# Optimization experiments

Measured on AMD Instinct MI355X. Metric: run time of the kernel, lower is better.

The kernel has to match this reference:

```python
import jax, jax.numpy as jnp
import numpy as np

N = 100000   # nodes
E = 1600000  # edges
IN = 41      # in_channels (21 atom + 20 residue)
ED = 8       # edge_dim
H = 64       # hidden_dim
L = 3        # num_layers
G = 256      # graphs in batch
ATOM = 21
EPS = 1e-5   # GraphNorm eps


def setup_inputs() -> dict:
    key = jax.random.key(0)
    ks = jax.random.split(key, 32)
    s = 0.1
    x = jax.random.normal(ks[0], (N, IN), jnp.float32)
    # make even-index nodes 'ligand' atoms (zero residue part) so both MLP branches fire
    lig = (jnp.arange(N) % 2) == 0
    x = x.at[:, ATOM:].set(jnp.where(lig[:, None], 0.0, x[:, ATOM:]))
    edge_index = jax.random.randint(ks[1], (2, E), 0, N)
    edge_attr = jax.random.normal(ks[2], (E, ED), jnp.float32)
    batch = jnp.sort(jax.random.randint(ks[3], (N,), 0, G))
    p = {
        "lig_W1": s * jax.random.normal(ks[4], (IN, H), jnp.float32),
        "lig_b1": jnp.zeros((H,), jnp.float32),
        "lig_W2": s * jax.random.normal(ks[5], (H, H), jnp.float32),
        "lig_b2": jnp.zeros((H,), jnp.float32),
        "prot_W1": s * jax.random.normal(ks[6], (IN, H), jnp.float32),
        "prot_b1": jnp.zeros((H,), jnp.float32),
        "prot_W2": s * jax.random.normal(ks[7], (H, H), jnp.float32),
        "prot_b2": jnp.zeros((H,), jnp.float32),
        # per-layer stacked params for the 3 GINEConv + GraphNorm blocks
        "conv_We": s * jax.random.normal(ks[8], (L, ED, H), jnp.float32),
        "conv_be": jnp.zeros((L, H), jnp.float32),
        "conv_W1": s * jax.random.normal(ks[9], (L, H, H), jnp.float32),
        "conv_b1": jnp.zeros((L, H), jnp.float32),
        "conv_W2": s * jax.random.normal(ks[10], (L, H, H), jnp.float32),
        "conv_b2": jnp.zeros((L, H), jnp.float32),
        "norm_w": jnp.ones((L, H), jnp.float32),
        "norm_b": jnp.zeros((L, H), jnp.float32),
        "norm_a": jnp.ones((L, H), jnp.float32),  # mean_scale alpha
        "out_W1": s * jax.random.normal(ks[11], (H, H), jnp.float32),
        "out_b1": jnp.zeros((H,), jnp.float32),
        "out_W2": s * jax.random.normal(ks[12], (H, 1), jnp.float32),
        "out_b2": jnp.zeros((1,), jnp.float32),
    }
    return dict(x=x, edge_index=edge_index, edge_attr=edge_attr, batch=batch, **p)


def reference(x, edge_index, edge_attr, batch,
              lig_W1, lig_b1, lig_W2, lig_b2,
              prot_W1, prot_b1, prot_W2, prot_b2,
              conv_We, conv_be, conv_W1, conv_b1, conv_W2, conv_b2,
              norm_w, norm_b, norm_a,
              out_W1, out_b1, out_W2, out_b2):
    # --- input encoder: ligand vs protein branch by residue-part mask ---
    res_mask = jnp.sum(jnp.abs(x[:, ATOM:]), axis=1) > 1e-6
    h_lig = jax.nn.relu(jax.nn.relu(x @ lig_W1 + lig_b1) @ lig_W2 + lig_b2)
    h_prot = jax.nn.relu(jax.nn.relu(x @ prot_W1 + prot_b1) @ prot_W2 + prot_b2)
    h = jnp.where(res_mask[:, None], h_prot, h_lig)  # [N, H]

    src, dst = edge_index[0], edge_index[1]
    counts = jnp.maximum(jax.ops.segment_sum(jnp.ones((N,), h.dtype), batch,
                                             num_segments=G), 1.0)[:, None]  # [G,1]

    for l in range(L):
        # GINEConv (eps=0): nn(h_i + sum_j relu(h_j + lin(e_ij)))
        e = edge_attr @ conv_We[l] + conv_be[l]           # [E, H]
        msg = jax.nn.relu(h[src] + e)                     # [E, H]
        aggr = jax.ops.segment_sum(msg, dst, num_segments=N)
        z = h + aggr
        h = jax.nn.relu(z @ conv_W1[l] + conv_b1[l]) @ conv_W2[l] + conv_b2[l]
        # GraphNorm: (h - alpha*mean_g) / sqrt(var_g + eps) * w + b
        mean = jax.ops.segment_sum(h, batch, num_segments=G) / counts  # [G, H]
        out = h - norm_a[l] * mean[batch]
        var = jax.ops.segment_sum(out * out, batch, num_segments=G) / counts
        h = norm_w[l] * (out / jnp.sqrt(var + EPS)[batch]) + norm_b[l]
        h = jax.nn.relu(h)

    # global_add_pool + readout (dropout = identity at eval)
    g = jax.ops.segment_sum(h, batch, num_segments=G)  # [G, H]
    out = jax.nn.relu(g @ out_W1 + out_b1) @ out_W2 + out_b2  # [G, 1]
    return out.reshape(-1)
```

## Files before the change

kernel.cpp:

```cpp
#include <hip/hip_runtime.h>

#define NN 100000
#define NE 1600000
#define IN_CH 41
#define EDIM 8
#define H 64
#define GNUM 256
#define ATOM 21
#define EPSV 1e-5f
#define EPW 16
#define NTILE (NN / 16)

#define BSH 7
#define BDST 128
#define NBK 782
#define GRP 16
#define BDST2 8
#define NAGG 12500
#define SCAP 3584

#define VPT_H 8
#define EPB_H (1024 * VPT_H)
#define NBLK_H ((NE + EPB_H - 1) / EPB_H)
#define VPT_P1 16
#define EPB_P1 (1024 * VPT_P1)
#define NBLK_P1 ((NE + EPB_P1 - 1) / EPB_P1)

typedef unsigned short u16;
typedef unsigned int u32;
typedef unsigned long long u64;
typedef __attribute__((ext_vector_type(8))) short short8;
typedef __attribute__((ext_vector_type(4))) float floatx4;

__device__ __forceinline__ u16 f2bf(float f) {
    u32 u = __float_as_uint(f);
    u32 r = (u + 0x7FFFu + ((u >> 16) & 1u)) >> 16;
    return (u16)r;
}
__device__ __forceinline__ float bf2f(u16 u) {
    return __uint_as_float(((u32)u) << 16);
}
__device__ __forceinline__ floatx4 mfma16(short8 a, short8 b, floatx4 c) {
    return __builtin_amdgcn_mfma_f32_16x16x32_bf16(a, b, c, 0, 0, 0);
}
__device__ __forceinline__ short8 pack_bf8(float4 a, float4 b) {
    short8 s;
    s[0] = (short)f2bf(a.x); s[1] = (short)f2bf(a.y);
    s[2] = (short)f2bf(a.z); s[3] = (short)f2bf(a.w);
    s[4] = (short)f2bf(b.x); s[5] = (short)f2bf(b.y);
    s[6] = (short)f2bf(b.z); s[7] = (short)f2bf(b.w);
    return s;
}

__global__ __launch_bounds__(256) void partition_kernel(
    const float* __restrict__ x, int* __restrict__ ctr,
    int* __restrict__ lig_list, int* __restrict__ prot_list)
{
    const int n = blockIdx.x * 256 + threadIdx.x;
    const int lane = threadIdx.x & 63;
    float m = 0.0f;
    if (n < NN) {
        const float* xr = x + (size_t)n * IN_CH + ATOM;
#pragma unroll
        for (int d = 0; d < IN_CH - ATOM; ++d) m += fabsf(xr[d]);
    }
    const bool valid = n < NN;
    const bool prot = valid && (m > 1e-6f);
    const bool lig = valid && !prot;

    const u64 bl = __ballot(lig);
    const u64 bp = __ballot(prot);
    const u64 below_m = (lane == 63) ? (~0ull >> 1) : ((1ull << lane) - 1ull);
    int base_l = 0, base_p = 0;
    if (lane == 0) {
        if (bl) base_l = atomicAdd(&ctr[0], (int)__popcll(bl));
        if (bp) base_p = atomicAdd(&ctr[1], (int)__popcll(bp));
    }
    base_l = __shfl(base_l, 0, 64);
    base_p = __shfl(base_p, 0, 64);
    if (lig)  lig_list [base_l + (int)__popcll(bl & below_m)] = n;
    if (prot) prot_list[base_p + (int)__popcll(bp & below_m)] = n;
}

__global__ __launch_bounds__(256) void xb_kernel(
    const float* __restrict__ x, u16* __restrict__ xb)
{
    const int id = blockIdx.x * 256 + threadIdx.x;
    if (id >= NN * H) return;
    const int n = id >> 6, d = id & 63;
    xb[id] = (d < IN_CH) ? f2bf(x[(size_t)n * IN_CH + d]) : (u16)0;
}

__global__ __launch_bounds__(256) void ea2b_kernel(
    const float* __restrict__ ea, uint4* __restrict__ eab16g)
{
    const int e = blockIdx.x * 256 + threadIdx.x;
    if (e >= NE) return;
    const float4* e4 = (const float4*)(ea + (size_t)e * EDIM);
    const float4 a = e4[0], b = e4[1];
    uint4 u;
    u.x = (u32)f2bf(a.x) | ((u32)f2bf(a.y) << 16);
    u.y = (u32)f2bf(a.z) | ((u32)f2bf(a.w) << 16);
    u.z = (u32)f2bf(b.x) | ((u32)f2bf(b.y) << 16);
    u.w = (u32)f2bf(b.z) | ((u32)f2bf(b.w) << 16);
    eab16g[e] = u;
}

__global__ __launch_bounds__(256) void prep_w_kernel(
    const float* __restrict__ ligW1, const float* __restrict__ ligW2,
    const float* __restrict__ protW1, const float* __restrict__ protW2,
    const float* __restrict__ convW1, const float* __restrict__ convW2,
    u16* __restrict__ wf)
{
    const int id = blockIdx.x * 256 + threadIdx.x;
    if (id >= 10 * 4096) return;
    const int j = id & 7, l = (id >> 3) & 63, t = (id >> 9) & 3;
    const int c = (id >> 11) & 1, mat = id >> 12;
    const int k = c * 32 + ((l >> 4) * 8) + j;
    const int n = t * 16 + (l & 15);
    const float* src; int K = 64;
    if (mat == 0)      { src = ligW1;  K = IN_CH; }
    else if (mat == 1) { src = ligW2; }
    else if (mat == 2) { src = protW1; K = IN_CH; }
    else if (mat == 3) { src = protW2; }
    else {
        const int layer = (mat - 4) >> 1;
        src = (((mat - 4) & 1) ? convW2 : convW1) + (size_t)layer * H * H;
    }
    wf[id] = (k < K) ? f2bf(src[(size_t)k * H + n]) : (u16)0;
}

__global__ __launch_bounds__(256) void enc_mfma_kernel(
    const int* __restrict__ list, const int* __restrict__ countPtr,
    const u16* __restrict__ xb,
    const u16* __restrict__ w1f, const u16* __restrict__ w2f,
    const float* __restrict__ bia1, const float* __restrict__ bia2,
    float* __restrict__ h, u16* __restrict__ h16)
{
    __shared__ __align__(16) u16 hid[4][16 * 72];
    const int wv = threadIdx.x >> 6;
    const int lane = threadIdx.x & 63;
    const int tile = blockIdx.x * 4 + wv;
    const int count = *countPtr;
    if (tile * 16 >= count) return;
    const int quad = lane >> 4;
    const int mi = lane & 15;
    int idx = tile * 16 + mi;
    if (idx >= count) idx = count - 1;
    const int nid = list[idx];

    const short8 a0 = *(const short8*)(xb + (size_t)nid * H + quad * 8);
    const short8 a1 = *(const short8*)(xb + (size_t)nid * H + 32 + quad * 8);

    floatx4 acc[4];
#pragma unroll
    for (int t = 0; t < 4; ++t) acc[t] = (floatx4){0.f, 0.f, 0.f, 0.f};
#pragma unroll
    for (int t = 0; t < 4; ++t) {
        const short8 b0 = *(const short8*)(w1f + ((size_t)(0 * 4 + t) * 64 + lane) * 8);
        const short8 b1 = *(const short8*)(w1f + ((size_t)(1 * 4 + t) * 64 + lane) * 8);
        acc[t] = mfma16(a0, b0, acc[t]);
        acc[t] = mfma16(a1, b1, acc[t]);
    }

    u16* myh = hid[wv];
#pragma unroll
    for (int t = 0; t < 4; ++t) {
        const float bv = bia1[t * 16 + mi];
#pragma unroll
        for (int r = 0; r < 4; ++r) {
            const float v = fmaxf(acc[t][r] + bv, 0.0f);
            myh[(quad * 4 + r) * 72 + t * 16 + mi] = f2bf(v);
        }
    }
    asm volatile("s_waitcnt lgkmcnt(0)" ::: "memory");

    const short8 c0 = *(const short8*)(myh + mi * 72 + quad * 8);
    const short8 c1 = *(const short8*)(myh + mi * 72 + 32 + quad * 8);

    floatx4 acc2[4];
#pragma unroll
    for (int t = 0; t < 4; ++t) acc2[t] = (floatx4){0.f, 0.f, 0.f, 0.f};
#pragma unroll
    for (int t = 0; t < 4; ++t) {
        const short8 b0 = *(const short8*)(w2f + ((size_t)(0 * 4 + t) * 64 + lane) * 8);
        const short8 b1 = *(const short8*)(w2f + ((size_t)(1 * 4 + t) * 64 + lane) * 8);
        acc2[t] = mfma16(c0, b0, acc2[t]);
        acc2[t] = mfma16(c1, b1, acc2[t]);
    }

#pragma unroll
    for (int t = 0; t < 4; ++t) {
        const float bv = bia2[t * 16 + mi];
#pragma unroll
        for (int r = 0; r < 4; ++r) {
            const int row = quad * 4 + r;
            const int nr = __shfl(nid, row, 64);
            if (tile * 16 + row < count) {
                const float v = fmaxf(acc2[t][r] + bv, 0.0f);
                h[(size_t)nr * H + t * 16 + mi] = v;
                h16[(size_t)nr * H + t * 16 + mi] = f2bf(v);
            }
        }
    }
}

__global__ __launch_bounds__(256) void mlp_mfma_kernel(
    const u16* __restrict__ w1f, const u16* __restrict__ w2f,
    const float* __restrict__ bia1, const float* __restrict__ bia2,
    float* __restrict__ h)
{
    __shared__ __align__(16) u16 hid[4][16 * 72];
    const int wv = threadIdx.x >> 6;
    const int lane = threadIdx.x & 63;
    const int tile = blockIdx.x * 4 + wv;
    if (tile >= NTILE) return;
    const int quad = lane >> 4;
    const int mi = lane & 15;
    const int row = tile * 16 + mi;
    const float* zr = h + (size_t)row * H;

    const float4 f0 = *(const float4*)(zr + quad * 8);
    const float4 f1 = *(const float4*)(zr + quad * 8 + 4);
    const float4 f2 = *(const float4*)(zr + 32 + quad * 8);
    const float4 f3 = *(const float4*)(zr + 32 + quad * 8 + 4);
    const short8 a0 = pack_bf8(f0, f1);
    const short8 a1 = pack_bf8(f2, f3);

    floatx4 acc[4];
#pragma unroll
    for (int t = 0; t < 4; ++t) acc[t] = (floatx4){0.f, 0.f, 0.f, 0.f};
#pragma unroll
    for (int t = 0; t < 4; ++t) {
        const short8 b0 = *(const short8*)(w1f + ((size_t)(0 * 4 + t) * 64 + lane) * 8);
        const short8 b1 = *(const short8*)(w1f + ((size_t)(1 * 4 + t) * 64 + lane) * 8);
        acc[t] = mfma16(a0, b0, acc[t]);
        acc[t] = mfma16(a1, b1, acc[t]);
    }

    u16* myh = hid[wv];
#pragma unroll
    for (int t = 0; t < 4; ++t) {
        const float bv = bia1[t * 16 + mi];
#pragma unroll
        for (int r = 0; r < 4; ++r) {
            const float v = fmaxf(acc[t][r] + bv, 0.0f);
            myh[(quad * 4 + r) * 72 + t * 16 + mi] = f2bf(v);
        }
    }
    asm volatile("s_waitcnt lgkmcnt(0)" ::: "memory");

    const short8 c0 = *(const short8*)(myh + mi * 72 + quad * 8);
    const short8 c1 = *(const short8*)(myh + mi * 72 + 32 + quad * 8);

    floatx4 acc2[4];
#pragma unroll
    for (int t = 0; t < 4; ++t) acc2[t] = (floatx4){0.f, 0.f, 0.f, 0.f};
#pragma unroll
    for (int t = 0; t < 4; ++t) {
        const short8 b0 = *(const short8*)(w2f + ((size_t)(0 * 4 + t) * 64 + lane) * 8);
        const short8 b1 = *(const short8*)(w2f + ((size_t)(1 * 4 + t) * 64 + lane) * 8);
        acc2[t] = mfma16(c0, b0, acc2[t]);
        acc2[t] = mfma16(c1, b1, acc2[t]);
    }

#pragma unroll
    for (int t = 0; t < 4; ++t) {
        const float bv = bia2[t * 16 + mi];
#pragma unroll
        for (int r = 0; r < 4; ++r) {
            const int orow = tile * 16 + quad * 4 + r;
            h[(size_t)orow * H + t * 16 + mi] = acc2[t][r] + bv;
        }
    }
}

__global__ void bounds_kernel(const int* __restrict__ batch, int* __restrict__ start)
{
    int g = blockIdx.x * blockDim.x + threadIdx.x;
    if (g > GNUM) return;
    int lo = 0, hi = NN;
    while (lo < hi) {
        int mid = (lo + hi) >> 1;
        if (batch[mid] < g) lo = mid + 1; else hi = mid;
    }
    start[g] = lo;
}

__global__ __launch_bounds__(1024) void bhist_kernel(
    const int* __restrict__ ei, int* __restrict__ gbcount)
{
    __shared__ int cnt[NBK];
    const int t = threadIdx.x;
    if (t < NBK) cnt[t] = 0;
    __syncthreads();
    const int base = blockIdx.x * EPB_H;
#pragma unroll
    for (int v = 0; v < VPT_H; ++v) {
        const int e = base + v * 1024 + t;
        if (e < NE) atomicAdd(&cnt[ei[NE + e] >> BSH], 1);
    }
    __syncthreads();
    if (t < NBK && cnt[t]) atomicAdd(&gbcount[t], cnt[t]);
}

__global__ __launch_bounds__(1024) void bscan_kernel(
    const int* __restrict__ gbcount, int* __restrict__ gstart, int* __restrict__ gcur)
{
    __shared__ int s[1024];
    const int t = threadIdx.x;
    int v = (t < NBK) ? gbcount[t] : 0;
    s[t] = v;
    __syncthreads();
#pragma unroll
    for (int off = 1; off < 1024; off <<= 1) {
        int tmp = (t >= off) ? s[t - off] : 0;
        __syncthreads();
        s[t] += tmp;
        __syncthreads();
    }
    if (t < NBK) { gstart[t] = s[t] - v; gcur[t] = s[t] - v; }
    if (t == 0) gstart[NBK] = NE;
}

__global__ __launch_bounds__(1024) void p1_kernel(
    const int* __restrict__ ei, int* __restrict__ gcur, int2* __restrict__ tmp)
{
    __shared__ int cnt[NBK];
    __shared__ int cur[NBK];
    const int t = threadIdx.x;
    if (t < NBK) cnt[t] = 0;
    __syncthreads();
    const int base = blockIdx.x * EPB_P1;
    int dstv[VPT_P1];
#pragma unroll
    for (int v = 0; v < VPT_P1; ++v) {
        const int e = base + v * 1024 + t;
        dstv[v] = -1;
        if (e < NE) {
            dstv[v] = ei[NE + e];
            atomicAdd(&cnt[dstv[v] >> BSH], 1);
        }
    }
    __syncthreads();
    if (t < NBK) cur[t] = cnt[t] ? atomicAdd(&gcur[t], cnt[t]) : 0;
    __syncthreads();
#pragma unroll
    for (int v = 0; v < VPT_P1; ++v) {
        const int e = base + v * 1024 + t;
        if (e < NE) {
            const int b = dstv[v] >> BSH;
            const int pos = atomicAdd(&cur[b], 1);
            tmp[pos] = make_int2(ei[e] | ((dstv[v] & (BDST - 1)) << 17), e);
        }
    }
}

__global__ __launch_bounds__(1024) void sort1_kernel(
    const int2* __restrict__ tmp, const uint4* __restrict__ eab16g,
    const int* __restrict__ gstart,
    u32* __restrict__ brec, uint4* __restrict__ bfeat, int* __restrict__ astart)
{
    __shared__ int hist[BDST];
    __shared__ int cursor[BDST];
    __shared__ __align__(8) int2 stage[SCAP];
    const int b = blockIdx.x;
    const int t = threadIdx.x;
    const int s = gstart[b], e = gstart[b + 1];
    const int cnt = e - s;

    if (t < BDST) hist[t] = 0;
    __syncthreads();
    for (int i = s + t; i < e; i += 1024)
        atomicAdd(&hist[(tmp[i].x >> 17) & (BDST - 1)], 1);
    __syncthreads();
    if (t < BDST) cursor[t] = hist[t];
    __syncthreads();
#pragma unroll
    for (int off = 1; off < BDST; off <<= 1) {
        int v = (t < BDST && t >= off) ? cursor[t - off] : 0;
        __syncthreads();
        if (t < BDST) cursor[t] += v;
        __syncthreads();
    }
    if (t < BDST) cursor[t] -= hist[t];
    __syncthreads();
    if (t < GRP) {
        const int a = b * GRP + t;
        if (a < NAGG) astart[a] = s + cursor[t * BDST2];
    }
    if (b == 0 && t == 0) astart[NAGG] = NE;

    if (cnt <= SCAP) {
        for (int i = s + t; i < e; i += 1024) {
            const int2 r = tmp[i];
            const int slot = atomicAdd(&cursor[(r.x >> 17) & (BDST - 1)], 1);
            stage[slot] = r;
        }
        __syncthreads();
        for (int i = t; i < cnt; i += 1024) {
            const int2 r = stage[i];
            brec[s + i] = (u32)r.x;
            bfeat[s + i] = eab16g[r.y];
        }
    } else {
        if (t < BDST) cursor[t] += s;
        __syncthreads();
        for (int i = s + t; i < e; i += 1024) {
            const int2 r = tmp[i];
            const int pos = atomicAdd(&cursor[(r.x >> 17) & (BDST - 1)], 1);
            brec[pos] = (u32)r.x;
            bfeat[pos] = eab16g[r.y];
        }
    }
}

__global__ __launch_bounds__(256, 4) void aggr_kernel(
    const u32* __restrict__ brec,
    const u32* __restrict__ bfeat32,
    const int* __restrict__ astart,
    const float* __restrict__ We, const float* __restrict__ be,
    const u16* __restrict__ h16, float* __restrict__ h)
{
    const int lane = threadIdx.x & 63;
    const int bk = blockIdx.x * 4 + (threadIdx.x >> 6);
    const int row0 = bk * BDST2;
    const int s = astart[bk], e = astart[bk + 1];
    if (s >= e) return;

    float we_r[EDIM];
#pragma unroll
    for (int d = 0; d < EDIM; ++d) we_r[d] = We[d * H + lane];
    const float be_r = be[lane];

    float acc = 0.0f;
    int cur = -1;

    for (int base = s; base < e; base += EPW) {
        const int cnt = min(EPW, e - base);
        u32 rec = 0;
        if ((lane & 15) < cnt) rec = brec[base + (lane & 15)];
        u32 eu = 0;
        if (lane < cnt * 4) eu = bfeat32[(size_t)base * 4 + lane];

        float hv[EPW];
#pragma unroll
        for (int j = 0; j < EPW; ++j) {
            const int sj = (int)(__builtin_amdgcn_readlane(rec, j) & 0x1ffffu);
            hv[j] = bf2f(h16[(size_t)sj * H + lane]);
        }
#pragma unroll
        for (int j = 0; j < EPW; ++j) {
            if (j < cnt) {
                const u32 rj = __builtin_amdgcn_readlane(rec, j);
                const int ld = (int)((rj >> 17) & (BDST2 - 1));
                float msg = be_r;
#pragma unroll
                for (int p = 0; p < 4; ++p) {
                    const u32 w2 = __builtin_amdgcn_readlane(eu, j * 4 + p);
                    msg = fmaf(__uint_as_float(w2 << 16), we_r[2 * p], msg);
                    msg = fmaf(__uint_as_float(w2 & 0xffff0000u), we_r[2 * p + 1], msg);
                }
                const float val = fmaxf(hv[j] + msg, 0.0f);
                if (ld != cur) {
                    if (cur >= 0)
                        unsafeAtomicAdd(&h[(size_t)(row0 + cur) * H + lane], acc);
                    acc = 0.0f;
                    cur = ld;
                }
                acc += val;
            }
        }
    }
    unsafeAtomicAdd(&h[(size_t)(row0 + cur) * H + lane], acc);
}

__global__ __launch_bounds__(1024) void graphnorm_kernel(
    float* __restrict__ h, u16* __restrict__ h16,
    const int* __restrict__ start,
    const float* __restrict__ w, const float* __restrict__ b,
    const float* __restrict__ a,
    float* __restrict__ pool, int do_pool)
{
    __shared__ float red1[16][H], red2[16][H];
    __shared__ float amean_s[H], rstd_s[H];
    const int g = blockIdx.x;
    const int lane = threadIdx.x & 63;
    const int wv = threadIdx.x >> 6;
    const int s = start[g], e = start[g + 1];

    float s1 = 0.f, s2 = 0.f;
    for (int i = s + wv; i < e; i += 16) {
        float v = h[(size_t)i * H + lane];
        s1 += v; s2 += v * v;
    }
    red1[wv][lane] = s1; red2[wv][lane] = s2;
    __syncthreads();
    if (threadIdx.x < H) {
        float t1 = 0.f, t2 = 0.f;
#pragma unroll
        for (int k = 0; k < 16; ++k) { t1 += red1[k][lane]; t2 += red2[k][lane]; }
        float cnt = fmaxf((float)(e - s), 1.0f);
        float mean = t1 / cnt;
        float alpha = a[lane];
        float var = t2 / cnt - (2.0f * alpha - alpha * alpha) * mean * mean;
        var = fmaxf(var, 0.0f);
        amean_s[lane] = alpha * mean;
        rstd_s[lane] = rsqrtf(var + EPSV);
    }
    __syncthreads();
    const float am = amean_s[lane], rstd = rstd_s[lane];
    const float ww = w[lane], bb = b[lane];
    float ps = 0.f;
    for (int i = s + wv; i < e; i += 16) {
        float v = (h[(size_t)i * H + lane] - am) * rstd * ww + bb;
        v = fmaxf(v, 0.0f);
        h[(size_t)i * H + lane] = v;
        h16[(size_t)i * H + lane] = f2bf(v);
        ps += v;
    }
    if (do_pool && e > s) unsafeAtomicAdd(&pool[g * H + lane], ps);
}

__global__ __launch_bounds__(64) void final_kernel(
    const float* __restrict__ pool,
    const float* __restrict__ W1, const float* __restrict__ b1,
    const float* __restrict__ W2, const float* __restrict__ b2,
    float* __restrict__ out)
{
    const int g = blockIdx.x;
    const int lane = threadIdx.x;
    const float gv = pool[g * H + lane];
    float acc = b1[lane];
#pragma unroll
    for (int d = 0; d < H; ++d)
        acc = fmaf(__shfl(gv, d, 64), W1[d * H + lane], acc);
    float r = fmaxf(acc, 0.0f);
    float v = r * W2[lane];
#pragma unroll
    for (int o = 32; o > 0; o >>= 1) v += __shfl_xor(v, o, 64);
    if (lane == 0) out[g] = v + b2[0];
}

extern "C" void kernel_launch(void* const* d_in, const int* in_sizes, int n_in,
                              void* d_out, int out_size, void* d_ws, size_t ws_size,
                              hipStream_t stream)
{
    const float* x      = (const float*)d_in[0];
    const int*   ei     = (const int*)  d_in[1];
    const float* ea     = (const float*)d_in[2];
    const int*   batch  = (const int*)  d_in[3];
    const float* ligW1  = (const float*)d_in[4];
    const float* ligb1  = (const float*)d_in[5];
    const float* ligW2  = (const float*)d_in[6];
    const float* ligb2  = (const float*)d_in[7];
    const float* protW1 = (const float*)d_in[8];
    const float* protb1 = (const float*)d_in[9];
    const float* protW2 = (const float*)d_in[10];
    const float* protb2 = (const float*)d_in[11];
    const float* convWe = (const float*)d_in[12];
    const float* convbe = (const float*)d_in[13];
    const float* convW1 = (const float*)d_in[14];
    const float* convb1 = (const float*)d_in[15];
    const float* convW2 = (const float*)d_in[16];
    const float* convb2 = (const float*)d_in[17];
    const float* normw  = (const float*)d_in[18];
    const float* normb  = (const float*)d_in[19];
    const float* norma  = (const float*)d_in[20];
    const float* outW1  = (const float*)d_in[21];
    const float* outb1  = (const float*)d_in[22];
    const float* outW2  = (const float*)d_in[23];
    const float* outb2  = (const float*)d_in[24];

    float* out = (float*)d_out;

    float* h         = (float*)d_ws;
    uint4* bfeat     = (uint4*)(h + (size_t)NN * H);
    u32*   brec      = (u32*)(bfeat + (size_t)NE);
    u16*   h16       = (u16*)(brec + (size_t)NE);
    u16*   xb        = h16 + (size_t)NN * H;
    u16*   wf        = xb + (size_t)NN * H;
    int2*  tmp       = (int2*)h;
    uint4* eab16g    = (uint4*)h16;

    int*   ctr       = (int*)(wf + 40960);
    int*   gbcount   = ctr + 2;
    float* pool      = (float*)(gbcount + NBK);
    int*   gstart    = (int*)(pool + GNUM * H);
    int*   gcur      = gstart + (NBK + 1);
    int*   astart    = gcur + NBK;
    int*   start     = astart + (NAGG + 1);
    int*   lig_list  = start + (GNUM + 1);
    int*   prot_list = lig_list + NN;

    hipMemsetAsync(ctr, 0, ((size_t)2 + NBK + GNUM * H) * sizeof(int), stream);

    prep_w_kernel<<<(10 * 4096 + 255) / 256, 256, 0, stream>>>(
        ligW1, ligW2, protW1, protW2, convW1, convW2, wf);
    partition_kernel<<<(NN + 255) / 256, 256, 0, stream>>>(x, ctr, lig_list, prot_list);
    bounds_kernel<<<2, 256, 0, stream>>>(batch, start);

    bhist_kernel<<<NBLK_H, 1024, 0, stream>>>(ei, gbcount);
    bscan_kernel<<<1, 1024, 0, stream>>>(gbcount, gstart, gcur);
    ea2b_kernel<<<(NE + 255) / 256, 256, 0, stream>>>(ea, eab16g);
    p1_kernel<<<NBLK_P1, 1024, 0, stream>>>(ei, gcur, tmp);
    sort1_kernel<<<NBK, 1024, 0, stream>>>(tmp, eab16g, gstart, brec, bfeat, astart);

    xb_kernel<<<(NN * H + 255) / 256, 256, 0, stream>>>(x, xb);
    const int enc_blocks = (NTILE + 3) / 4;
    enc_mfma_kernel<<<enc_blocks, 256, 0, stream>>>(
        lig_list, &ctr[0], xb, wf + 0 * 4096, wf + 1 * 4096, ligb1, ligb2, h, h16);
    enc_mfma_kernel<<<enc_blocks, 256, 0, stream>>>(
        prot_list, &ctr[1], xb, wf + 2 * 4096, wf + 3 * 4096, protb1, protb2, h, h16);

    const int aggr_blocks = NAGG / 4;
    const int mlp_blocks = (NTILE + 3) / 4;
    for (int l = 0; l < 3; ++l) {
        aggr_kernel<<<aggr_blocks, 256, 0, stream>>>(
            brec, (const u32*)bfeat, astart,
            convWe + (size_t)l * EDIM * H, convbe + (size_t)l * H, h16, h);
        mlp_mfma_kernel<<<mlp_blocks, 256, 0, stream>>>(
            wf + (size_t)(4 + 2 * l) * 4096, wf + (size_t)(5 + 2 * l) * 4096,
            convb1 + (size_t)l * H, convb2 + (size_t)l * H, h);
        graphnorm_kernel<<<GNUM, 1024, 0, stream>>>(
            h, h16, start, normw + (size_t)l * H, normb + (size_t)l * H,
            norma + (size_t)l * H, pool, (l == 2) ? 1 : 0);
    }
    final_kernel<<<GNUM, 64, 0, stream>>>(pool, outW1, outb1, outW2, outb2, out);
}
```

Before: 635.3 us.

## Fuse edge-attr bf16 packing into sort, split aggr loop into full/tail chunks

```diff
diff --git a/kernel.cpp b/kernel.cpp
--- a/kernel.cpp
+++ b/kernel.cpp
@@ -51,6 +51,16 @@
     s[6] = (short)f2bf(b.z); s[7] = (short)f2bf(b.w);
     return s;
 }
+__device__ __forceinline__ uint4 pack_ea(const float* __restrict__ ea, int eid) {
+    const float4* e4 = (const float4*)(ea + (size_t)eid * EDIM);
+    const float4 a = e4[0], b = e4[1];
+    uint4 u;
+    u.x = (u32)f2bf(a.x) | ((u32)f2bf(a.y) << 16);
+    u.y = (u32)f2bf(a.z) | ((u32)f2bf(a.w) << 16);
+    u.z = (u32)f2bf(b.x) | ((u32)f2bf(b.y) << 16);
+    u.w = (u32)f2bf(b.z) | ((u32)f2bf(b.w) << 16);
+    return u;
+}
 
 __global__ __launch_bounds__(256) void partition_kernel(
     const float* __restrict__ x, int* __restrict__ ctr,
@@ -89,21 +99,6 @@
     if (id >= NN * H) return;
     const int n = id >> 6, d = id & 63;
     xb[id] = (d < IN_CH) ? f2bf(x[(size_t)n * IN_CH + d]) : (u16)0;
-}
-
-__global__ __launch_bounds__(256) void ea2b_kernel(
-    const float* __restrict__ ea, uint4* __restrict__ eab16g)
-{
-    const int e = blockIdx.x * 256 + threadIdx.x;
-    if (e >= NE) return;
-    const float4* e4 = (const float4*)(ea + (size_t)e * EDIM);
-    const float4 a = e4[0], b = e4[1];
-    uint4 u;
-    u.x = (u32)f2bf(a.x) | ((u32)f2bf(a.y) << 16);
-    u.y = (u32)f2bf(a.z) | ((u32)f2bf(a.w) << 16);
-    u.z = (u32)f2bf(b.x) | ((u32)f2bf(b.y) << 16);
-    u.w = (u32)f2bf(b.z) | ((u32)f2bf(b.w) << 16);
-    eab16g[e] = u;
 }
 
 __global__ __launch_bounds__(256) void prep_w_kernel(
@@ -357,7 +352,7 @@
 }
 
 __global__ __launch_bounds__(1024) void sort1_kernel(
-    const int2* __restrict__ tmp, const uint4* __restrict__ eab16g,
+    const int2* __restrict__ tmp, const float* __restrict__ ea,
     const int* __restrict__ gstart,
     u32* __restrict__ brec, uint4* __restrict__ bfeat, int* __restrict__ astart)
 {
@@ -401,7 +396,7 @@
         for (int i = t; i < cnt; i += 1024) {
             const int2 r = stage[i];
             brec[s + i] = (u32)r.x;
-            bfeat[s + i] = eab16g[r.y];
+            bfeat[s + i] = pack_ea(ea, r.y);
         }
     } else {
         if (t < BDST) cursor[t] += s;
@@ -410,12 +405,12 @@
             const int2 r = tmp[i];
             const int pos = atomicAdd(&cursor[(r.x >> 17) & (BDST - 1)], 1);
             brec[pos] = (u32)r.x;
-            bfeat[pos] = eab16g[r.y];
-        }
-    }
-}
-
-__global__ __launch_bounds__(256, 4) void aggr_kernel(
+            bfeat[pos] = pack_ea(ea, r.y);
+        }
+    }
+}
+
+__global__ __launch_bounds__(256) void aggr_kernel(
     const u32* __restrict__ brec,
     const u32* __restrict__ bfeat32,
     const int* __restrict__ astart,
@@ -436,8 +431,41 @@
     float acc = 0.0f;
     int cur = -1;
 
-    for (int base = s; base < e; base += EPW) {
-        const int cnt = min(EPW, e - base);
+    const int nfull = (e - s) / EPW;
+    int base = s;
+    for (int c = 0; c < nfull; ++c, base += EPW) {
+        const u32 rec = brec[base + (lane & 15)];
+        const u32 eu = bfeat32[(size_t)base * 4 + lane];
+
+        float hv[EPW];
+#pragma unroll
+        for (int j = 0; j < EPW; ++j) {
+            const int sj = (int)(__builtin_amdgcn_readlane(rec, j) & 0x1ffffu);
+            hv[j] = bf2f(h16[(size_t)sj * H + lane]);
+        }
+#pragma unroll
+        for (int j = 0; j < EPW; ++j) {
+            const u32 rj = __builtin_amdgcn_readlane(rec, j);
+            const int ld = (int)((rj >> 17) & (BDST2 - 1));
+            float msg = be_r;
+#pragma unroll
+            for (int p = 0; p < 4; ++p) {
+                const u32 w2 = __builtin_amdgcn_readlane(eu, j * 4 + p);
+                msg = fmaf(__uint_as_float(w2 << 16), we_r[2 * p], msg);
+                msg = fmaf(__uint_as_float(w2 & 0xffff0000u), we_r[2 * p + 1], msg);
+            }
+            const float val = fmaxf(hv[j] + msg, 0.0f);
+            if (ld != cur) {
+                if (cur >= 0)
+                    unsafeAtomicAdd(&h[(size_t)(row0 + cur) * H + lane], acc);
+                acc = 0.0f;
+                cur = ld;
+            }
+            acc += val;
+        }
+    }
+    if (base < e) {
+        const int cnt = e - base;
         u32 rec = 0;
         if ((lane & 15) < cnt) rec = brec[base + (lane & 15)];
         u32 eu = 0;
@@ -581,7 +609,6 @@
     u16*   xb        = h16 + (size_t)NN * H;
     u16*   wf        = xb + (size_t)NN * H;
     int2*  tmp       = (int2*)h;
-    uint4* eab16g    = (uint4*)h16;
 
     int*   ctr       = (int*)(wf + 40960);
     int*   gbcount   = ctr + 2;
@@ -602,9 +629,8 @@
 
     bhist_kernel<<<NBLK_H, 1024, 0, stream>>>(ei, gbcount);
     bscan_kernel<<<1, 1024, 0, stream>>>(gbcount, gstart, gcur);
-    ea2b_kernel<<<(NE + 255) / 256, 256, 0, stream>>>(ea, eab16g);
     p1_kernel<<<NBLK_P1, 1024, 0, stream>>>(ei, gcur, tmp);
-    sort1_kernel<<<NBK, 1024, 0, stream>>>(tmp, eab16g, gstart, brec, bfeat, astart);
+    sort1_kernel<<<NBK, 1024, 0, stream>>>(tmp, ea, gstart, brec, bfeat, astart);
 
     xb_kernel<<<(NN * H + 255) / 256, 256, 0, stream>>>(x, xb);
     const int enc_blocks = (NTILE + 3) / 4;
```

Result: faster. 603.3 us (-5.0%).
